# Kernel optimization log

Measured on AMD Instinct MI355X. Metric: run time of the kernel, lower is better.

## Reference

```python
import jax, jax.numpy as jnp
import numpy as np

ALPHA = 1.0
NUM_SEGMENTS = 50000  # number of structures (segments)


def setup_inputs() -> dict:
    key = jax.random.key(0)
    k1, k2, k3 = jax.random.split(key, 3)
    n, d = 1000000, 128
    prop = jax.random.normal(k1, (1, n, d), dtype=jnp.float32)
    weights = jax.random.uniform(k2, (1, n), dtype=jnp.float32)
    index = jnp.sort(jax.random.randint(k3, (1, n), 0, NUM_SEGMENTS, dtype=jnp.int32))
    return {"prop": prop, "weights": weights, "index": index}


def reference(prop, weights, index):
    # result_s = sum_{i in segment s} w_i^alpha * prop_i / sum_{i in s} w_i^alpha
    expo_w = weights ** ALPHA                      # [1, n]
    idx = index.reshape(-1)                        # [n]
    weighted = prop * expo_w[:, :, None]           # [1, n, d]
    prop_sum = jax.ops.segment_sum(weighted[0], idx, num_segments=NUM_SEGMENTS)[None]   # [1, S, d]
    weight_sum = jax.ops.segment_sum(expo_w[0], idx, num_segments=NUM_SEGMENTS)[None]   # [1, S]
    return prop_sum / weight_sum[:, :, None]
```

## Files before the change

### kernel.cpp

```cpp
#include <hip/hip_runtime.h>
#include <hip/hip_bf16.h>

#define NUM_SEGMENTS 50000

typedef float f32x4 __attribute__((ext_vector_type(4)));

__device__ __forceinline__ f32x4 ntload4(const f32x4* p) {
    return __builtin_nontemporal_load(p);
}
__device__ __forceinline__ void ntstore4(f32x4* p, f32x4 v) {
    __builtin_nontemporal_store(v, p);
}

__global__ void build_starts_v4(const int4* __restrict__ idx4,
                                const int*  __restrict__ idx,
                                int* __restrict__ starts,
                                int n4, int n, int S) {
    int i4 = blockIdx.x * blockDim.x + threadIdx.x;
    if (i4 >= n4) return;
    int4 v = idx4[i4];
    int base = i4 * 4;
    int prev = (base == 0) ? -1 : idx[base - 1];
    int a0 = v.x, a1 = v.y, a2 = v.z, a3 = v.w;
    for (int s = prev + 1; s <= a0; ++s) starts[s] = base;
    for (int s = a0 + 1;  s <= a1; ++s) starts[s] = base + 1;
    for (int s = a1 + 1;  s <= a2; ++s) starts[s] = base + 2;
    for (int s = a2 + 1;  s <= a3; ++s) starts[s] = base + 3;
    if (base + 4 >= n) {
        for (int s = a3 + 1; s <= S; ++s) starts[s] = n;
    }
}

__global__ void build_starts_tail(const int* __restrict__ idx,
                                  int* __restrict__ starts,
                                  int n4, int n, int S) {
    int i = n4 * 4 + blockIdx.x * blockDim.x + threadIdx.x;
    if (i >= n) return;
    int cur = idx[i];
    int prev = (i == 0) ? -1 : idx[i - 1];
    for (int s = prev + 1; s <= cur; ++s) starts[s] = i;
    if (i == n - 1)
        for (int s = cur + 1; s <= S; ++s) starts[s] = n;
}

__device__ __forceinline__ void accum_seg(const f32x4* __restrict__ prop4,
                                          const float* __restrict__ w,
                                          int start, int nrows,
                                          int col4, int rg,
                                          f32x4& acc, float& wsum) {
    const f32x4* p  = prop4 + (size_t)(start + rg) * 32 + col4;
    const float* wp = w + start;
    int r = rg;
    for (; r + 4 < nrows; r += 8) {
        float w0 = wp[r], w1 = wp[r + 4];
        f32x4 p0 = ntload4(p), p1 = ntload4(p + 128);
        p += 256;
        acc += p0 * w0;
        acc += p1 * w1;
        wsum += w0 + w1;
    }
    for (; r < nrows; r += 4) {
        float w0 = wp[r];
        f32x4 p0 = ntload4(p);
        p += 128;
        acc += p0 * w0;
        wsum += w0;
    }
}

__global__ void __launch_bounds__(128)
seg_weighted_avg_d128(const f32x4* __restrict__ prop4,
                      const float* __restrict__ w,
                      const int*   __restrict__ starts,
                      f32x4*       __restrict__ out4) {
    const int s0  = blockIdx.x * 2;
    const int st0 = starts[s0];
    const int st1 = starts[s0 + 1];
    const int st2 = starts[s0 + 2];

    const int t    = threadIdx.x;
    const int col4 = t & 31;
    const int rg   = t >> 5;

    f32x4 accA = (f32x4)0.f, accB = (f32x4)0.f;
    float wsA = 0.f, wsB = 0.f;

    accum_seg(prop4, w, st0, st1 - st0, col4, rg, accA, wsA);
    accum_seg(prop4, w, st1, st2 - st1, col4, rg, accB, wsB);

    __shared__ f32x4 laccA[128], laccB[128];
    __shared__ float lwA[128], lwB[128];
    laccA[t] = accA; laccB[t] = accB;
    lwA[t]   = wsA;  lwB[t]   = wsB;
    __syncthreads();

    if (t < 64) {
        const f32x4* lacc = (t < 32) ? laccA : laccB;
        const float* lw   = (t < 32) ? lwA   : lwB;
        const int u = t & 31;
        f32x4 a = (lacc[u] + lacc[u + 32]) + (lacc[u + 64] + lacc[u + 96]);
        float ws = (lw[u] + lw[u + 32]) + (lw[u + 64] + lw[u + 96]);
        ntstore4((f32x4*)&out4[(size_t)(s0 + (t >> 5)) * 32 + u], a / ws);
    }
}

__global__ void __launch_bounds__(128)
seg_weighted_avg_generic(const float* __restrict__ prop,
                         const float* __restrict__ w,
                         const int*   __restrict__ starts,
                         float*       __restrict__ out,
                         int d) {
    const int s     = blockIdx.x;
    const int start = starts[s];
    const int end   = starts[s + 1];
    const int t     = threadIdx.x;
    const float* p  = prop + (size_t)start * d + t;
    float acc = 0.f, wsum = 0.f;
    for (int i = start; i < end; ++i) {
        float wi = w[i];
        wsum += wi;
        acc = fmaf(wi, p[0], acc);
        p += d;
    }
    out[(size_t)s * d + t] = acc / wsum;
}

extern "C" void kernel_launch(void* const* d_in, const int* in_sizes, int n_in,
                              void* d_out, int out_size, void* d_ws, size_t ws_size,
                              hipStream_t stream) {
    const float* prop = (const float*)d_in[0];
    const float* w    = (const float*)d_in[1];
    const int*   idx  = (const int*)d_in[2];
    float* out        = (float*)d_out;

    const int n = in_sizes[1];
    const int d = in_sizes[0] / in_sizes[1];
    const int S = NUM_SEGMENTS;

    int* starts = (int*)d_ws;

    const int n4 = n / 4;
    build_starts_v4<<<(n4 + 255) / 256, 256, 0, stream>>>(
        (const int4*)idx, idx, starts, n4, n, S);
    if (n % 4) {
        build_starts_tail<<<((n - n4 * 4) + 255) / 256, 256, 0, stream>>>(
            idx, starts, n4, n, S);
    }

    if (d == 128 && (S % 2) == 0) {
        seg_weighted_avg_d128<<<S / 2, 128, 0, stream>>>(
            (const f32x4*)prop, w, starts, (f32x4*)out);
    } else {
        seg_weighted_avg_generic<<<S, d, 0, stream>>>(prop, w, starts, out, d);
    }
}
```

Before: 96.53 us.

## Replace segment-start prepass with in-kernel binary search on sorted index

Drops the separate build_starts kernels that scanned the whole index array and wrote a starts table. Each block now finds its segment boundaries itself by binary search over the sorted index, starting from a window around the proportional guess s*n/S and falling back to a full-range search if the boundary lies outside it. This removes one kernel launch and a full read of the 4 MB index plus the starts writes. In exchange, each block pays a serialized chain of dependent global loads before its main accumulation can start.

```diff
diff --git a/kernel.cpp b/kernel.cpp
--- a/kernel.cpp
+++ b/kernel.cpp
@@ -12,35 +12,26 @@
     __builtin_nontemporal_store(v, p);
 }
 
-__global__ void build_starts_v4(const int4* __restrict__ idx4,
-                                const int*  __restrict__ idx,
-                                int* __restrict__ starts,
-                                int n4, int n, int S) {
-    int i4 = blockIdx.x * blockDim.x + threadIdx.x;
-    if (i4 >= n4) return;
-    int4 v = idx4[i4];
-    int base = i4 * 4;
-    int prev = (base == 0) ? -1 : idx[base - 1];
-    int a0 = v.x, a1 = v.y, a2 = v.z, a3 = v.w;
-    for (int s = prev + 1; s <= a0; ++s) starts[s] = base;
-    for (int s = a0 + 1;  s <= a1; ++s) starts[s] = base + 1;
-    for (int s = a1 + 1;  s <= a2; ++s) starts[s] = base + 2;
-    for (int s = a2 + 1;  s <= a3; ++s) starts[s] = base + 3;
-    if (base + 4 >= n) {
-        for (int s = a3 + 1; s <= S; ++s) starts[s] = n;
+__device__ __forceinline__ int lb_range(const int* __restrict__ idx,
+                                        int lo, int hi, int s) {
+    while (lo < hi) {
+        int mid = (lo + hi) >> 1;
+        if (idx[mid] < s) lo = mid + 1; else hi = mid;
     }
+    return lo;
 }
 
-__global__ void build_starts_tail(const int* __restrict__ idx,
-                                  int* __restrict__ starts,
-                                  int n4, int n, int S) {
-    int i = n4 * 4 + blockIdx.x * blockDim.x + threadIdx.x;
-    if (i >= n) return;
-    int cur = idx[i];
-    int prev = (i == 0) ? -1 : idx[i - 1];
-    for (int s = prev + 1; s <= cur; ++s) starts[s] = i;
-    if (i == n - 1)
-        for (int s = cur + 1; s <= S; ++s) starts[s] = n;
+__device__ __forceinline__ int lb_guess(const int* __restrict__ idx,
+                                        int n, int S, int s) {
+    if (s <= 0) return 0;
+    if (s >= S) return n;
+    long long g = (long long)s * n / S;
+    int lo = (int)g - 6144; if (lo < 0) lo = 0;
+    int hi = (int)g + 6144; if (hi > n) hi = n;
+    int r = lb_range(idx, lo, hi, s);
+    if (r == lo && lo > 0 && idx[r - 1] >= s)      r = lb_range(idx, 0, lo, s);
+    else if (r == hi && hi < n && idx[r] < s)      r = lb_range(idx, hi, n, s);
+    return r;
 }
 
 __device__ __forceinline__ void accum_seg(const f32x4* __restrict__ prop4,
@@ -71,14 +62,17 @@
 __global__ void __launch_bounds__(128)
 seg_weighted_avg_d128(const f32x4* __restrict__ prop4,
                       const float* __restrict__ w,
-                      const int*   __restrict__ starts,
-                      f32x4*       __restrict__ out4) {
-    const int s0  = blockIdx.x * 2;
-    const int st0 = starts[s0];
-    const int st1 = starts[s0 + 1];
-    const int st2 = starts[s0 + 2];
+                      const int*   __restrict__ idx,
+                      f32x4*       __restrict__ out4,
+                      int n, int S) {
+    const int s0 = blockIdx.x * 2;
+    const int t  = threadIdx.x;
 
-    const int t    = threadIdx.x;
+    __shared__ int sb[3];
+    if (t < 3) sb[t] = lb_guess(idx, n, S, s0 + t);
+    __syncthreads();
+    const int st0 = sb[0], st1 = sb[1], st2 = sb[2];
+
     const int col4 = t & 31;
     const int rg   = t >> 5;
 
@@ -107,13 +101,15 @@
 __global__ void __launch_bounds__(128)
 seg_weighted_avg_generic(const float* __restrict__ prop,
                          const float* __restrict__ w,
-                         const int*   __restrict__ starts,
+                         const int*   __restrict__ idx,
                          float*       __restrict__ out,
-                         int d) {
-    const int s     = blockIdx.x;
-    const int start = starts[s];
-    const int end   = starts[s + 1];
-    const int t     = threadIdx.x;
+                         int n, int S, int d) {
+    const int s = blockIdx.x;
+    const int t = threadIdx.x;
+    __shared__ int sb[2];
+    if (t < 2) sb[t] = lb_guess(idx, n, S, s + t);
+    __syncthreads();
+    const int start = sb[0], end = sb[1];
     const float* p  = prop + (size_t)start * d + t;
     float acc = 0.f, wsum = 0.f;
     for (int i = start; i < end; ++i) {
@@ -137,20 +133,10 @@
     const int d = in_sizes[0] / in_sizes[1];
     const int S = NUM_SEGMENTS;
 
-    int* starts = (int*)d_ws;
-
-    const int n4 = n / 4;
-    build_starts_v4<<<(n4 + 255) / 256, 256, 0, stream>>>(
-        (const int4*)idx, idx, starts, n4, n, S);
-    if (n % 4) {
-        build_starts_tail<<<((n - n4 * 4) + 255) / 256, 256, 0, stream>>>(
-            idx, starts, n4, n, S);
-    }
-
     if (d == 128 && (S % 2) == 0) {
         seg_weighted_avg_d128<<<S / 2, 128, 0, stream>>>(
-            (const f32x4*)prop, w, starts, (f32x4*)out);
+            (const f32x4*)prop, w, idx, (f32x4*)out, n, S);
     } else {
-        seg_weighted_avg_generic<<<S, d, 0, stream>>>(prop, w, starts, out, d);
+        seg_weighted_avg_generic<<<S, d, 0, stream>>>(prop, w, idx, out, n, S, d);
     }
 }
```

Result: slower. 107.8 us (+11.7%).
